# Kernel tuning notes

Hardware: AMD Instinct MI355X
Metric: run time of the kernel (lower is better)

Reference implementation:

```python
import jax, jax.numpy as jnp
from jax import lax
import numpy as np

D_MODEL = 1024
D_STATE = 16
D_CONV = 4
EXPAND = 2
D_INNER = EXPAND * D_MODEL
BATCH = 2
SEQLEN = 1024


def setup_inputs() -> dict:
    key = jax.random.key(0)
    ks = jax.random.split(key, 8)
    x = jax.random.normal(ks[0], (BATCH, SEQLEN, D_MODEL), jnp.float32)
    W_in = jax.random.normal(ks[1], (2 * D_INNER, D_MODEL), jnp.float32) * (1.0 / np.sqrt(D_MODEL))
    conv_w = jax.random.normal(ks[2], (D_INNER, 1, D_CONV), jnp.float32) * (1.0 / np.sqrt(D_CONV))
    conv_b = jax.random.normal(ks[3], (D_INNER,), jnp.float32) * 0.02
    W_x = jax.random.normal(ks[4], (2 * D_STATE, D_INNER), jnp.float32) * (1.0 / np.sqrt(D_INNER))
    W_dt = jax.random.normal(ks[5], (D_INNER, D_INNER), jnp.float32) * (1.0 / np.sqrt(D_INNER))
    b_dt = jax.random.normal(ks[6], (D_INNER,), jnp.float32) * 0.02
    # A_log = log(arange(1..d_state)) repeated over d_inner rows, as in __init__
    A_log = jnp.log(jnp.tile(jnp.arange(1, D_STATE + 1, dtype=jnp.float32), (D_INNER, 1)))
    D = jnp.ones((D_INNER,), jnp.float32)
    W_out = jax.random.normal(ks[7], (D_MODEL, D_INNER), jnp.float32) * (1.0 / np.sqrt(D_INNER))
    return {"x": x, "W_in": W_in, "conv_w": conv_w, "conv_b": conv_b,
            "W_x": W_x, "W_dt": W_dt, "b_dt": b_dt, "A_log": A_log,
            "D": D, "W_out": W_out}


def reference(x, W_in, conv_w, conv_b, W_x, W_dt, b_dt, A_log, D, W_out):
    d_inner, _, d_conv = conv_w.shape
    d_state = A_log.shape[1]

    # in_proj and split into x / gate z
    xz = x @ W_in.T                                   # (B, L, 2*d_inner)
    xi, z = jnp.split(xz, 2, axis=-1)

    # causal depthwise conv1d: torch pads both sides by d_conv-1 then slices
    # [:seqlen], which equals left-only padding of d_conv-1
    xc = lax.conv_general_dilated(
        xi.transpose(0, 2, 1), conv_w, window_strides=(1,),
        padding=[(d_conv - 1, 0)],
        dimension_numbers=("NCH", "OIH", "NCH"),
        feature_group_count=d_inner)
    xc = xc + conv_b[None, :, None]
    u = jax.nn.silu(xc.transpose(0, 2, 1))            # (B, L, d_inner)

    # input-dependent B, C and dt
    BC = u @ W_x.T                                    # (B, L, 2*d_state)
    Bmat, Cmat = jnp.split(BC, 2, axis=-1)
    dt = jax.nn.softplus(u @ W_dt.T + b_dt)           # (B, L, d_inner)

    A = -jnp.exp(A_log)                               # (d_inner, d_state)
    dA = jnp.exp(dt[..., None] * A)                   # (B, L, d_inner, d_state)
    dBu = dt[..., None] * Bmat[:, :, None, :] * u[..., None]

    def step(s, inp):
        dA_t, dBu_t, C_t = inp
        s = dA_t * s + dBu_t                          # (B, d_inner, d_state)
        y_t = jnp.einsum("bdn,bn->bd", s, C_t)
        return s, y_t

    s0 = jnp.zeros((x.shape[0], d_inner, d_state), x.dtype)
    _, ys = lax.scan(step, s0,
                     (dA.transpose(1, 0, 2, 3),
                      dBu.transpose(1, 0, 2, 3),
                      Cmat.transpose(1, 0, 2)))
    y = ys.transpose(1, 0, 2) + D * u                 # (B, L, d_inner)

    y = y * jax.nn.silu(z)
    # dropout is identity in eval mode
    return y @ W_out.T
```

## Files before the change

### kernel.cpp

```cpp
#include <hip/hip_runtime.h>
#include <hip/hip_bf16.h>
#include <math.h>

#define B_SZ   2
#define LSEQ   1024
#define DMODEL 1024
#define DSTATE 16
#define DCONV  4
#define DINNER 2048
#define MROWS  (B_SZ * LSEQ)
#define NCHUNK 32
#define TCHUNK (LSEQ / NCHUNK)
#define NCAT   2176
#define BKS    64

typedef __attribute__((ext_vector_type(8))) short bf16x8;
typedef __attribute__((ext_vector_type(4))) float f32x4;

__device__ __forceinline__ void gl2lds16(const void* g, void* l) {
    __builtin_amdgcn_global_load_lds(
        (const __attribute__((address_space(1))) void*)g,
        (__attribute__((address_space(3))) void*)l, 16, 0, 0);
}

__device__ __forceinline__ void cvt8(const float* __restrict__ in,
                                     __hip_bfloat16* __restrict__ out, int i)
{
    float4 a = *(const float4*)&in[i];
    float4 b = *(const float4*)&in[i + 4];
    union { __hip_bfloat16 h[8]; int4 v; } o;
    o.h[0] = __float2bfloat16(a.x); o.h[1] = __float2bfloat16(a.y);
    o.h[2] = __float2bfloat16(a.z); o.h[3] = __float2bfloat16(a.w);
    o.h[4] = __float2bfloat16(b.x); o.h[5] = __float2bfloat16(b.y);
    o.h[6] = __float2bfloat16(b.z); o.h[7] = __float2bfloat16(b.w);
    *(int4*)&out[i] = o.v;
}

__global__ __launch_bounds__(256)
void cvt_all(const float* __restrict__ x,    __hip_bfloat16* __restrict__ xb,
             const float* __restrict__ win,  __hip_bfloat16* __restrict__ winb,
             const float* __restrict__ wdt,  const float* __restrict__ wx,
             __hip_bfloat16* __restrict__ wcat,
             const float* __restrict__ wout, __hip_bfloat16* __restrict__ woutb)
{
    const int b = blockIdx.x;
    const int t8 = threadIdx.x * 8;
    if      (b < 1024) cvt8(x,    xb,    b * 2048 + t8);
    else if (b < 3072) cvt8(win,  winb,  (b - 1024) * 2048 + t8);
    else if (b < 5120) cvt8(wdt,  wcat,  (b - 3072) * 2048 + t8);
    else if (b < 5152) cvt8(wx,   wcat + (size_t)DINNER * DINNER,
                                         (b - 5120) * 2048 + t8);
    else               cvt8(wout, woutb, (b - 5152) * 2048 + t8);
}

template<int EPI>
__global__ __launch_bounds__(256)
void gemm_bt(const __hip_bfloat16* __restrict__ A,
             const __hip_bfloat16* __restrict__ B,
             const float* __restrict__ bias,
             float* __restrict__ Cbase, size_t pstride, int ldc,
             float* __restrict__ C2,
             int K, int klen)
{
    constexpr int BN   = 64;
    constexpr int NLD  = (128 + BN) / 8 / 4;
    constexpr int SMEL = (128 + BN) * BKS;
    __shared__ __hip_bfloat16 sm[2 * SMEL];

    const int tid  = threadIdx.x;
    const int lane = tid & 63;
    const int w    = tid >> 6;
    const int m0 = blockIdx.x * 128;
    const int n0 = blockIdx.y * BN;
    const int wr = w >> 1, wc = w & 1;
    const int kbase = blockIdx.z * klen;
    float* __restrict__ C = Cbase + (size_t)blockIdx.z * pstride;

    const int lrow = lane >> 3;
    const int swc  = ((lane & 7) ^ lrow) * 8;
    const __hip_bfloat16* srcp[NLD];
    #pragma unroll
    for (int i = 0; i < NLD; ++i) {
        const int q = w + 4 * i;
        srcp[i] = (q < 16)
            ? A + (size_t)(m0 + q * 8 + lrow) * K + kbase + swc
            : B + (size_t)(n0 + (q - 16) * 8 + lrow) * K + kbase + swc;
    }

    f32x4 acc[4][2] = {};
    const int l7 = lane & 7, l15 = lane & 15, lq = lane >> 4;
    const int sw0 = (lq ^ l7) * 8;
    const int sw1 = sw0 ^ 32;

    #pragma unroll
    for (int i = 0; i < NLD; ++i)
        gl2lds16(srcp[i], sm + (w + 4 * i) * 512);
    asm volatile("s_waitcnt vmcnt(0)" ::: "memory");
    __builtin_amdgcn_s_barrier();
    __builtin_amdgcn_sched_barrier(0);

    const int nt = klen / BKS;
    int buf = 0;
    for (int t = 0; t < nt; ++t) {
        if (t + 1 < nt) {
            #pragma unroll
            for (int i = 0; i < NLD; ++i)
                gl2lds16(srcp[i] + (size_t)(t + 1) * BKS,
                         sm + (buf ^ 1) * SMEL + (w + 4 * i) * 512);
        }
        const __hip_bfloat16* As = sm + buf * SMEL;
        const __hip_bfloat16* Bs = As + 128 * BKS;
        bf16x8 a0[4], a1[4], b0[2], b1[2];
        #pragma unroll
        for (int m = 0; m < 4; ++m) {
            const int r = (wr * 64 + m * 16 + l15) * BKS;
            a0[m] = *(const bf16x8*)&As[r + sw0];
            a1[m] = *(const bf16x8*)&As[r + sw1];
        }
        #pragma unroll
        for (int n = 0; n < 2; ++n) {
            const int r = (wc * 32 + n * 16 + l15) * BKS;
            b0[n] = *(const bf16x8*)&Bs[r + sw0];
            b1[n] = *(const bf16x8*)&Bs[r + sw1];
        }
        #pragma unroll
        for (int m = 0; m < 4; ++m)
            #pragma unroll
            for (int n = 0; n < 2; ++n) {
                acc[m][n] = __builtin_amdgcn_mfma_f32_16x16x32_bf16(
                    a0[m], b0[n], acc[m][n], 0, 0, 0);
                acc[m][n] = __builtin_amdgcn_mfma_f32_16x16x32_bf16(
                    a1[m], b1[n], acc[m][n], 0, 0, 0);
            }
        asm volatile("s_waitcnt vmcnt(0)" ::: "memory");
        __builtin_amdgcn_s_barrier();
        __builtin_amdgcn_sched_barrier(0);
        buf ^= 1;
    }

    #pragma unroll
    for (int m = 0; m < 4; ++m)
        #pragma unroll
        for (int n = 0; n < 2; ++n) {
            const int col = n0 + wc * 32 + n * 16 + l15;
            #pragma unroll
            for (int j = 0; j < 4; ++j) {
                const int row = m0 + wr * 64 + m * 16 + lq * 4 + j;
                float v = acc[m][n][j];
                if (EPI == 0) {
                    C[(size_t)row * ldc + col] = v;
                } else {
                    if (col < DINNER) {
                        v += bias[col];
                        v = (v > 20.f) ? v : log1pf(__expf(v));
                        C[(size_t)row * ldc + col] = v;
                    } else if (col < DINNER + 32) {
                        C2[(size_t)row * 32 + (col - DINNER)] = v;
                    }
                }
            }
        }
}

__global__ __launch_bounds__(256)
void add2(const float* __restrict__ a, const float* __restrict__ b,
          float* __restrict__ o)
{
    int i = (blockIdx.x * 256 + threadIdx.x) * 4;
    float4 va = *(const float4*)&a[i];
    float4 vb = *(const float4*)&b[i];
    va.x += vb.x; va.y += vb.y; va.z += vb.z; va.w += vb.w;
    *(float4*)&o[i] = va;
}

__global__ __launch_bounds__(256)
void conv_silu(const float* __restrict__ xz, const float* __restrict__ cw,
               const float* __restrict__ cb, __hip_bfloat16* __restrict__ u_bf)
{
    int idx = blockIdx.x * blockDim.x + threadIdx.x;
    int d = idx & (DINNER - 1);
    int m = idx >> 11;
    int t = m & (LSEQ - 1);
    float acc = cb[d];
    #pragma unroll
    for (int j = 0; j < DCONV; ++j) {
        int tt = t - (DCONV - 1) + j;
        if (tt >= 0)
            acc += xz[(size_t)(m - t + tt) * 4096 + d] * cw[d * DCONV + j];
    }
    float v = acc / (1.f + __expf(-acc));
    u_bf[(size_t)m * DINNER + d] = __float2bfloat16(v);
}

__global__ __launch_bounds__(256)
void scan_part1(const float* __restrict__ dt, const __hip_bfloat16* __restrict__ u,
                const float* __restrict__ bc, const float* __restrict__ A_log,
                float* __restrict__ s_end, float* __restrict__ dtsum)
{
    const int d = blockIdx.x * 256 + threadIdx.x;
    const int c = blockIdx.y;
    const int b = blockIdx.z;
    __shared__ float bcs[TCHUNK][32];
    {
        int f = threadIdx.x * 4;
        const float* src = bc + ((size_t)b * LSEQ + c * TCHUNK) * 32;
        *(float4*)&bcs[f >> 5][f & 31] = *(const float4*)&src[f];
    }
    float An[16];
    {
        float4 a0 = *(const float4*)&A_log[d * DSTATE + 0];
        float4 a1 = *(const float4*)&A_log[d * DSTATE + 4];
        float4 a2 = *(const float4*)&A_log[d * DSTATE + 8];
        float4 a3 = *(const float4*)&A_log[d * DSTATE + 12];
        An[0]=-__expf(a0.x); An[1]=-__expf(a0.y); An[2]=-__expf(a0.z); An[3]=-__expf(a0.w);
        An[4]=-__expf(a1.x); An[5]=-__expf(a1.y); An[6]=-__expf(a1.z); An[7]=-__expf(a1.w);
        An[8]=-__expf(a2.x); An[9]=-__expf(a2.y); An[10]=-__expf(a2.z); An[11]=-__expf(a2.w);
        An[12]=-__expf(a3.x); An[13]=-__expf(a3.y); An[14]=-__expf(a3.z); An[15]=-__expf(a3.w);
    }
    __syncthreads();
    const float* dtp = dt + ((size_t)b * LSEQ + c * TCHUNK) * DINNER + d;
    const __hip_bfloat16* up = u + ((size_t)b * LSEQ + c * TCHUNK) * DINNER + d;
    float s[16] = {};
    float sum = 0.f;
    for (int t = 0; t < TCHUNK; ++t) {
        float dtv = dtp[(size_t)t * DINNER];
        float uv  = __bfloat162float(up[(size_t)t * DINNER]);
        sum += dtv;
        float du = dtv * uv;
        #pragma unroll
        for (int n = 0; n < 16; ++n) {
            float a = __expf(dtv * An[n]);
            s[n] = a * s[n] + du * bcs[t][n];
        }
    }
    float* se = s_end + ((size_t)(b * NCHUNK + c) * DINNER + d) * 16;
    #pragma unroll
    for (int q = 0; q < 4; ++q)
        *(float4*)&se[q * 4] = make_float4(s[q*4], s[q*4+1], s[q*4+2], s[q*4+3]);
    dtsum[(size_t)(b * NCHUNK + c) * DINNER + d] = sum;
}

__global__ __launch_bounds__(256)
void scan_combine(float* __restrict__ s_end, const float* __restrict__ dtsum,
                  const float* __restrict__ A_log)
{
    int idx = blockIdx.x * 256 + threadIdx.x;
    int n = idx & 15;
    int d = (idx >> 4) & (DINNER - 1);
    int b = idx >> 15;
    float An = -__expf(A_log[d * DSTATE + n]);
    float s = 0.f;
    for (int c = 0; c < NCHUNK; ++c) {
        size_t base = (size_t)(b * NCHUNK + c) * DINNER + d;
        float se = s_end[base * 16 + n];
        s_end[base * 16 + n] = s;
        float P = __expf(An * dtsum[base]);
        s = P * s + se;
    }
}

__global__ __launch_bounds__(256)
void scan_part2(const float* __restrict__ dt, const __hip_bfloat16* __restrict__ u,
                const float* __restrict__ bc, const float* __restrict__ s_in,
                const float* __restrict__ A_log, const float* __restrict__ Dp,
                const float* __restrict__ xz, __hip_bfloat16* __restrict__ y_bf)
{
    const int d = blockIdx.x * 256 + threadIdx.x;
    const int c = blockIdx.y;
    const int b = blockIdx.z;
    __shared__ float bcs[TCHUNK][32];
    {
        int f = threadIdx.x * 4;
        const float* src = bc + ((size_t)b * LSEQ + c * TCHUNK) * 32;
        *(float4*)&bcs[f >> 5][f & 31] = *(const float4*)&src[f];
    }
    float An[16];
    {
        float4 a0 = *(const float4*)&A_log[d * DSTATE + 0];
        float4 a1 = *(const float4*)&A_log[d * DSTATE + 4];
        float4 a2 = *(const float4*)&A_log[d * DSTATE + 8];
        float4 a3 = *(const float4*)&A_log[d * DSTATE + 12];
        An[0]=-__expf(a0.x); An[1]=-__expf(a0.y); An[2]=-__expf(a0.z); An[3]=-__expf(a0.w);
        An[4]=-__expf(a1.x); An[5]=-__expf(a1.y); An[6]=-__expf(a1.z); An[7]=-__expf(a1.w);
        An[8]=-__expf(a2.x); An[9]=-__expf(a2.y); An[10]=-__expf(a2.z); An[11]=-__expf(a2.w);
        An[12]=-__expf(a3.x); An[13]=-__expf(a3.y); An[14]=-__expf(a3.z); An[15]=-__expf(a3.w);
    }
    float s[16];
    {
        const float* si = s_in + ((size_t)(b * NCHUNK + c) * DINNER + d) * 16;
        #pragma unroll
        for (int q = 0; q < 4; ++q) {
            float4 v = *(const float4*)&si[q * 4];
            s[q*4] = v.x; s[q*4+1] = v.y; s[q*4+2] = v.z; s[q*4+3] = v.w;
        }
    }
    const float Dd = Dp[d];
    __syncthreads();
    const float* dtp = dt + ((size_t)b * LSEQ + c * TCHUNK) * DINNER + d;
    const __hip_bfloat16* up = u + ((size_t)b * LSEQ + c * TCHUNK) * DINNER + d;
    const float* zp  = xz + ((size_t)b * LSEQ + c * TCHUNK) * 4096 + 2048 + d;
    __hip_bfloat16* yp = y_bf + ((size_t)b * LSEQ + c * TCHUNK) * DINNER + d;
    for (int t = 0; t < TCHUNK; ++t) {
        float dtv = dtp[(size_t)t * DINNER];
        float uv  = __bfloat162float(up[(size_t)t * DINNER]);
        float du = dtv * uv;
        float y = Dd * uv;
        #pragma unroll
        for (int n = 0; n < 16; ++n) {
            float a = __expf(dtv * An[n]);
            s[n] = a * s[n] + du * bcs[t][n];
            y += s[n] * bcs[t][16 + n];
        }
        float zv = zp[(size_t)t * 4096];
        yp[(size_t)t * DINNER] = __float2bfloat16(y * (zv / (1.f + __expf(-zv))));
    }
}

extern "C" void kernel_launch(void* const* d_in, const int* in_sizes, int n_in,
                              void* d_out, int out_size, void* d_ws, size_t ws_size,
                              hipStream_t stream)
{
    const float* x      = (const float*)d_in[0];
    const float* W_in   = (const float*)d_in[1];
    const float* conv_w = (const float*)d_in[2];
    const float* conv_b = (const float*)d_in[3];
    const float* W_x    = (const float*)d_in[4];
    const float* W_dt   = (const float*)d_in[5];
    const float* b_dt   = (const float*)d_in[6];
    const float* A_log  = (const float*)d_in[7];
    const float* Dp     = (const float*)d_in[8];
    const float* W_out  = (const float*)d_in[9];
    float* out = (float*)d_out;

    const size_t MB = 1ull << 20;
    char* w8 = (char*)d_ws;
    float* xz    = (float*)(w8);
    float* p3    = (float*)(w8);
    __hip_bfloat16* u_bf = (__hip_bfloat16*)(w8 + 32*MB);
    float* dtc   = (float*)(w8 + 40*MB);
    float* bc    = (float*)(w8 + 56*MB);
    float* sbuf  = (float*)(w8 + 57*MB);
    float* dtsum = (float*)(w8 + 65*MB);
    __hip_bfloat16* x_bf   = (__hip_bfloat16*)(w8 + 66*MB);
    __hip_bfloat16* Win_bf = (__hip_bfloat16*)(w8 + 70*MB);
    __hip_bfloat16* y_bf   = (__hip_bfloat16*)(w8 + 66*MB);
    __hip_bfloat16* Wcat_bf= (__hip_bfloat16*)(w8 + 78*MB);
    __hip_bfloat16* Wout_bf= (__hip_bfloat16*)(w8 + 86*MB + 512*1024);

    cvt_all<<<6176, 256, 0, stream>>>(x, x_bf, W_in, Win_bf,
                                      W_dt, W_x, Wcat_bf, W_out, Wout_bf);
    gemm_bt<0><<<dim3(16, 64, 1), 256, 0, stream>>>(
        x_bf, Win_bf, nullptr, xz, 0, 4096, nullptr, DMODEL, DMODEL);
    conv_silu<<<(MROWS * DINNER) / 256, 256, 0, stream>>>(xz, conv_w, conv_b, u_bf);
    gemm_bt<2><<<dim3(16, NCAT / 64, 1), 256, 0, stream>>>(
        u_bf, Wcat_bf, b_dt, dtc, 0, DINNER, bc, DINNER, DINNER);
    scan_part1<<<dim3(DINNER/256, NCHUNK, B_SZ), 256, 0, stream>>>(
        dtc, u_bf, bc, A_log, sbuf, dtsum);
    scan_combine<<<(B_SZ * DINNER * DSTATE) / 256, 256, 0, stream>>>(
        sbuf, dtsum, A_log);
    scan_part2<<<dim3(DINNER/256, NCHUNK, B_SZ), 256, 0, stream>>>(
        dtc, u_bf, bc, sbuf, A_log, Dp, xz, y_bf);
    gemm_bt<0><<<dim3(16, 16, 2), 256, 0, stream>>>(
        y_bf, Wout_bf, nullptr, p3, (size_t)MROWS * DMODEL, DMODEL, nullptr,
        DINNER, DINNER / 2);
    add2<<<(MROWS * DMODEL) / 1024, 256, 0, stream>>>(
        p3, p3 + (size_t)MROWS * DMODEL, out);
}
```

Measured before the change: 184.0 us.

## Triple-buffer GEMM LDS pipeline and store dt as bf16

```diff
diff --git a/kernel.cpp b/kernel.cpp
--- a/kernel.cpp
+++ b/kernel.cpp
@@ -59,13 +59,13 @@
              const __hip_bfloat16* __restrict__ B,
              const float* __restrict__ bias,
              float* __restrict__ Cbase, size_t pstride, int ldc,
-             float* __restrict__ C2,
+             __hip_bfloat16* __restrict__ Cb, float* __restrict__ C2,
              int K, int klen)
 {
     constexpr int BN   = 64;
     constexpr int NLD  = (128 + BN) / 8 / 4;
     constexpr int SMEL = (128 + BN) * BKS;
-    __shared__ __hip_bfloat16 sm[2 * SMEL];
+    __shared__ __hip_bfloat16 sm[3 * SMEL];
 
     const int tid  = threadIdx.x;
     const int lane = tid & 63;
@@ -92,23 +92,29 @@
     const int sw0 = (lq ^ l7) * 8;
     const int sw1 = sw0 ^ 32;
 
+    const int nt = klen / BKS;
     #pragma unroll
     for (int i = 0; i < NLD; ++i)
         gl2lds16(srcp[i], sm + (w + 4 * i) * 512);
-    asm volatile("s_waitcnt vmcnt(0)" ::: "memory");
-    __builtin_amdgcn_s_barrier();
-    __builtin_amdgcn_sched_barrier(0);
-
-    const int nt = klen / BKS;
-    int buf = 0;
+    if (nt > 1)
+        #pragma unroll
+        for (int i = 0; i < NLD; ++i)
+            gl2lds16(srcp[i] + BKS, sm + SMEL + (w + 4 * i) * 512);
+
+    int cb = 0;
     for (int t = 0; t < nt; ++t) {
-        if (t + 1 < nt) {
+        if (t + 1 < nt) asm volatile("s_waitcnt vmcnt(6)" ::: "memory");
+        else            asm volatile("s_waitcnt vmcnt(0)" ::: "memory");
+        __builtin_amdgcn_s_barrier();
+        __builtin_amdgcn_sched_barrier(0);
+        if (t + 2 < nt) {
+            int db = cb + 2; if (db >= 3) db -= 3;
             #pragma unroll
             for (int i = 0; i < NLD; ++i)
-                gl2lds16(srcp[i] + (size_t)(t + 1) * BKS,
-                         sm + (buf ^ 1) * SMEL + (w + 4 * i) * 512);
-        }
-        const __hip_bfloat16* As = sm + buf * SMEL;
+                gl2lds16(srcp[i] + (size_t)(t + 2) * BKS,
+                         sm + db * SMEL + (w + 4 * i) * 512);
+        }
+        const __hip_bfloat16* As = sm + cb * SMEL;
         const __hip_bfloat16* Bs = As + 128 * BKS;
         bf16x8 a0[4], a1[4], b0[2], b1[2];
         #pragma unroll
@@ -132,10 +138,7 @@
                 acc[m][n] = __builtin_amdgcn_mfma_f32_16x16x32_bf16(
                     a1[m], b1[n], acc[m][n], 0, 0, 0);
             }
-        asm volatile("s_waitcnt vmcnt(0)" ::: "memory");
-        __builtin_amdgcn_s_barrier();
-        __builtin_amdgcn_sched_barrier(0);
-        buf ^= 1;
+        cb = (cb == 2) ? 0 : cb + 1;
     }
 
     #pragma unroll
@@ -153,7 +156,7 @@
                     if (col < DINNER) {
                         v += bias[col];
                         v = (v > 20.f) ? v : log1pf(__expf(v));
-                        C[(size_t)row * ldc + col] = v;
+                        Cb[(size_t)row * ldc + col] = __float2bfloat16(v);
                     } else if (col < DINNER + 32) {
                         C2[(size_t)row * 32 + (col - DINNER)] = v;
                     }
@@ -193,7 +196,8 @@
 }
 
 __global__ __launch_bounds__(256)
-void scan_part1(const float* __restrict__ dt, const __hip_bfloat16* __restrict__ u,
+void scan_part1(const __hip_bfloat16* __restrict__ dt,
+                const __hip_bfloat16* __restrict__ u,
                 const float* __restrict__ bc, const float* __restrict__ A_log,
                 float* __restrict__ s_end, float* __restrict__ dtsum)
 {
@@ -218,13 +222,13 @@
         An[12]=-__expf(a3.x); An[13]=-__expf(a3.y); An[14]=-__expf(a3.z); An[15]=-__expf(a3.w);
     }
     __syncthreads();
-    const float* dtp = dt + ((size_t)b * LSEQ + c * TCHUNK) * DINNER + d;
-    const __hip_bfloat16* up = u + ((size_t)b * LSEQ + c * TCHUNK) * DINNER + d;
+    const __hip_bfloat16* dtp = dt + ((size_t)b * LSEQ + c * TCHUNK) * DINNER + d;
+    const __hip_bfloat16* up  = u  + ((size_t)b * LSEQ + c * TCHUNK) * DINNER + d;
     float s[16] = {};
     float sum = 0.f;
     for (int t = 0; t < TCHUNK; ++t) {
-        float dtv = dtp[(size_t)t * DINNER];
-        float uv  = __bfloat162float(up[(size_t)t * DINNER]);
+        float dtv = __bfloat162float(dtp[(size_t)t * DINNER]);
+        float uv  = __bfloat162float(up [(size_t)t * DINNER]);
         sum += dtv;
         float du = dtv * uv;
         #pragma unroll
@@ -260,7 +264,8 @@
 }
 
 __global__ __launch_bounds__(256)
-void scan_part2(const float* __restrict__ dt, const __hip_bfloat16* __restrict__ u,
+void scan_part2(const __hip_bfloat16* __restrict__ dt,
+                const __hip_bfloat16* __restrict__ u,
                 const float* __restrict__ bc, const float* __restrict__ s_in,
                 const float* __restrict__ A_log, const float* __restrict__ Dp,
                 const float* __restrict__ xz, __hip_bfloat16* __restrict__ y_bf)
@@ -296,13 +301,13 @@
     }
     const float Dd = Dp[d];
     __syncthreads();
-    const float* dtp = dt + ((size_t)b * LSEQ + c * TCHUNK) * DINNER + d;
-    const __hip_bfloat16* up = u + ((size_t)b * LSEQ + c * TCHUNK) * DINNER + d;
+    const __hip_bfloat16* dtp = dt + ((size_t)b * LSEQ + c * TCHUNK) * DINNER + d;
+    const __hip_bfloat16* up  = u  + ((size_t)b * LSEQ + c * TCHUNK) * DINNER + d;
     const float* zp  = xz + ((size_t)b * LSEQ + c * TCHUNK) * 4096 + 2048 + d;
     __hip_bfloat16* yp = y_bf + ((size_t)b * LSEQ + c * TCHUNK) * DINNER + d;
     for (int t = 0; t < TCHUNK; ++t) {
-        float dtv = dtp[(size_t)t * DINNER];
-        float uv  = __bfloat162float(up[(size_t)t * DINNER]);
+        float dtv = __bfloat162float(dtp[(size_t)t * DINNER]);
+        float uv  = __bfloat162float(up [(size_t)t * DINNER]);
         float du = dtv * uv;
         float y = Dd * uv;
         #pragma unroll
@@ -336,24 +341,24 @@
     char* w8 = (char*)d_ws;
     float* xz    = (float*)(w8);
     float* p3    = (float*)(w8);
-    __hip_bfloat16* u_bf = (__hip_bfloat16*)(w8 + 32*MB);
-    float* dtc   = (float*)(w8 + 40*MB);
-    float* bc    = (float*)(w8 + 56*MB);
-    float* sbuf  = (float*)(w8 + 57*MB);
-    float* dtsum = (float*)(w8 + 65*MB);
-    __hip_bfloat16* x_bf   = (__hip_bfloat16*)(w8 + 66*MB);
-    __hip_bfloat16* Win_bf = (__hip_bfloat16*)(w8 + 70*MB);
-    __hip_bfloat16* y_bf   = (__hip_bfloat16*)(w8 + 66*MB);
-    __hip_bfloat16* Wcat_bf= (__hip_bfloat16*)(w8 + 78*MB);
-    __hip_bfloat16* Wout_bf= (__hip_bfloat16*)(w8 + 86*MB + 512*1024);
+    __hip_bfloat16* u_bf  = (__hip_bfloat16*)(w8 + 32*MB);
+    __hip_bfloat16* dtc   = (__hip_bfloat16*)(w8 + 40*MB);
+    float* bc    = (float*)(w8 + 48*MB);
+    float* sbuf  = (float*)(w8 + 49*MB);
+    float* dtsum = (float*)(w8 + 57*MB);
+    __hip_bfloat16* x_bf   = (__hip_bfloat16*)(w8 + 58*MB);
+    __hip_bfloat16* Win_bf = (__hip_bfloat16*)(w8 + 62*MB);
+    __hip_bfloat16* y_bf   = (__hip_bfloat16*)(w8 + 58*MB);
+    __hip_bfloat16* Wcat_bf= (__hip_bfloat16*)(w8 + 70*MB);
+    __hip_bfloat16* Wout_bf= (__hip_bfloat16*)(w8 + 78*MB + 512*1024);
 
     cvt_all<<<6176, 256, 0, stream>>>(x, x_bf, W_in, Win_bf,
                                       W_dt, W_x, Wcat_bf, W_out, Wout_bf);
     gemm_bt<0><<<dim3(16, 64, 1), 256, 0, stream>>>(
-        x_bf, Win_bf, nullptr, xz, 0, 4096, nullptr, DMODEL, DMODEL);
+        x_bf, Win_bf, nullptr, xz, 0, 4096, nullptr, nullptr, DMODEL, DMODEL);
     conv_silu<<<(MROWS * DINNER) / 256, 256, 0, stream>>>(xz, conv_w, conv_b, u_bf);
     gemm_bt<2><<<dim3(16, NCAT / 64, 1), 256, 0, stream>>>(
-        u_bf, Wcat_bf, b_dt, dtc, 0, DINNER, bc, DINNER, DINNER);
+        u_bf, Wcat_bf, b_dt, nullptr, 0, DINNER, dtc, bc, DINNER, DINNER);
     scan_part1<<<dim3(DINNER/256, NCHUNK, B_SZ), 256, 0, stream>>>(
         dtc, u_bf, bc, A_log, sbuf, dtsum);
     scan_combine<<<(B_SZ * DINNER * DSTATE) / 256, 256, 0, stream>>>(
@@ -362,7 +367,7 @@
         dtc, u_bf, bc, sbuf, A_log, Dp, xz, y_bf);
     gemm_bt<0><<<dim3(16, 16, 2), 256, 0, stream>>>(
         y_bf, Wout_bf, nullptr, p3, (size_t)MROWS * DMODEL, DMODEL, nullptr,
-        DINNER, DINNER / 2);
+        nullptr, DINNER, DINNER / 2);
     add2<<<(MROWS * DMODEL) / 1024, 256, 0, stream>>>(
         p3, p3 + (size_t)MROWS * DMODEL, out);
 }
```

Measured after the change: 184.3 us. About the same (+0.2%).
